# Optimization experiments

Hardware: AMD Instinct MI355X
Metric: run time of the kernel (lower is better)

## Reference

```python
import jax, jax.numpy as jnp
import numpy as np

N, E = 50000, 800000
F_IN, HID, CLS, K = 128, 128, 40, 4


def setup_inputs() -> dict:
    key = jax.random.key(0)
    ks = jax.random.split(key, 6)
    x = jax.random.normal(ks[0], (N, F_IN), jnp.float32)
    edge_src = jax.random.randint(ks[1], (E,), 0, N, jnp.int32)
    edge_dst = jax.random.randint(ks[2], (E,), 0, N, jnp.int32)
    glorot = lambda k, sh, fan: jax.random.normal(k, sh, jnp.float32) * np.float32(1.0 / np.sqrt(fan))
    W0 = glorot(ks[3], (K, F_IN, HID), F_IN)
    W1 = glorot(ks[4], (K, HID, HID), HID)
    W2 = glorot(ks[5], (K, HID, CLS), HID)
    b0 = jnp.zeros((HID,), jnp.float32)
    b1 = jnp.zeros((HID,), jnp.float32)
    b2 = jnp.zeros((CLS,), jnp.float32)
    return dict(x=x, edge_src=edge_src, edge_dst=edge_dst,
                W0=W0, b0=b0, W1=W1, b1=b1, W2=W2, b2=b2)


def _cheb_edge_norm(edge_src, edge_dst, n):
    # PyG ChebConv 'sym' norm with lambda_max=2: scaled Laplacian
    # L_hat = 2L/lambda_max - I = -D^{-1/2} A D^{-1/2}  (diagonal is exactly 0)
    ones = jnp.ones(edge_src.shape[0], jnp.float32)
    deg = jax.ops.segment_sum(ones, edge_src, num_segments=n)
    dinv = jnp.where(deg > 0, jax.lax.rsqrt(jnp.maximum(deg, 1.0)), 0.0)
    return -dinv[edge_src] * dinv[edge_dst]  # [E]


def _cheb_conv(x, edge_src, edge_dst, w_norm, W, b, n):
    # Chebyshev recurrence: Tx0 = x, Tx1 = L_hat x, Tx_k = 2 L_hat Tx_{k-1} - Tx_{k-2}
    def lhat(t):  # SpMM: out[dst] += w * t[src]
        return jax.ops.segment_sum(t[edge_src] * w_norm[:, None], edge_dst, num_segments=n)

    Tx0 = x
    out = Tx0 @ W[0]
    Tx1 = lhat(Tx0)
    out = out + Tx1 @ W[1]
    for k in range(2, W.shape[0]):
        Tx2 = 2.0 * lhat(Tx1) - Tx0
        out = out + Tx2 @ W[k]
        Tx0, Tx1 = Tx1, Tx2
    return out + b


def reference(x, edge_src, edge_dst, W0, b0, W1, b1, W2, b2):
    n = x.shape[0]
    w_norm = _cheb_edge_norm(edge_src, edge_dst, n)
    h = x
    x1 = h
    for W, b in ((W0, b0), (W1, b1), (W2, b2)):
        x1 = _cheb_conv(h, edge_src, edge_dst, w_norm, W, b, n)
        h = jax.nn.relu(x1)  # dropout(p=0.6) is identity in eval mode
    # original returns log_softmax of the LAST conv's pre-activation x1
    return jax.nn.log_softmax(x1, axis=1)
```

## Files before the change

kernel.cpp:

```cpp
#include <hip/hip_runtime.h>
#include <math.h>

#define NN 50000
#define NE 800000
#define FDIM 128
#define CLS 40
#define AW 512
#define RSLOT 64

typedef __attribute__((ext_vector_type(8))) short short8v;
typedef __attribute__((ext_vector_type(8))) unsigned short ushort8v;
typedef __attribute__((ext_vector_type(4))) float f32x4;

__device__ inline float b2f(unsigned short u) {
    union { unsigned int i; float f; } v; v.i = ((unsigned)u) << 16; return v.f;
}
__device__ inline unsigned short f2b(float f) {
    unsigned int x = __float_as_uint(f);
    unsigned int r = (x + 0x7fffu + ((x >> 16) & 1u)) >> 16;
    return (unsigned short)r;
}


__global__ void zero_k(int* degi, int* fill) {
    int i = blockIdx.x * blockDim.x + threadIdx.x;
    if (i < NN) { degi[i] = 0; fill[i] = 0; }
}

#define NB_COUNT 782
#define NB_CVT   3125
#define NB_WH    256
#define NB_WO    96

__global__ __launch_bounds__(256) void prep_k(
        const int4* __restrict__ esrc4,
        int* degi,
        const float* __restrict__ x, unsigned short* __restrict__ Ab,
        const float* __restrict__ W0, const float* __restrict__ W1,
        const float* __restrict__ W2,
        unsigned short* __restrict__ Wt0, unsigned short* __restrict__ Wt1,
        unsigned short* __restrict__ Wt2) {
    int b = blockIdx.x;
    int tid = threadIdx.x;
    if (b < NB_COUNT) {
        int e = b * 256 + tid;
        if (e < NE / 4) {
            int4 s = esrc4[e];
            atomicAdd(&degi[s.x], 1); atomicAdd(&degi[s.y], 1);
            atomicAdd(&degi[s.z], 1); atomicAdd(&degi[s.w], 1);
        }
    } else if (b < NB_COUNT + NB_CVT) {
        int i = (b - NB_COUNT) * 256 + tid;
        int row = i >> 4, cg = i & 15;
        const float4* xp = (const float4*)(x + (size_t)row * FDIM + cg * 8);
        float4 v0 = xp[0], v1 = xp[1];
        ushort8v r;
        r[0] = f2b(v0.x); r[1] = f2b(v0.y); r[2] = f2b(v0.z); r[3] = f2b(v0.w);
        r[4] = f2b(v1.x); r[5] = f2b(v1.y); r[6] = f2b(v1.z); r[7] = f2b(v1.w);
        *(ushort8v*)(Ab + (size_t)row * AW + cg * 8) = r;
    } else if (b < NB_COUNT + NB_CVT + 2 * NB_WH) {
        int wi = b - NB_COUNT - NB_CVT;
        const float* W = (wi < NB_WH) ? W0 : W1;
        unsigned short* Wfm = (wi < NB_WH) ? Wt0 : Wt1;
        int i = (wi % NB_WH) * 256 + tid;
        int j = i & 7, l = (i >> 3) & 63, kcl = (i >> 9) & 3, nt = (i >> 11) & 7, c = i >> 14;
        int r = kcl * 32 + (l >> 4) * 8 + j;
        int col = nt * 16 + (l & 15);
        Wfm[i] = f2b(W[((size_t)c * 128 + r) * 128 + col]);
    } else {
        int i = (b - NB_COUNT - NB_CVT - 2 * NB_WH) * 256 + tid;
        int j = i & 7, l = (i >> 3) & 63, kc = (i >> 9) & 15, nt = i >> 13;
        int k = kc * 32 + (l >> 4) * 8 + j;
        int col = nt * 16 + (l & 15);
        int c = k >> 7, r = k & 127;
        float v = (col < CLS) ? W2[((size_t)c * 128 + r) * CLS + col] : 0.0f;
        Wt2[i] = f2b(v);
    }
}

__global__ void dinv_k(const int* __restrict__ degi, float* __restrict__ dinv) {
    int i = blockIdx.x * blockDim.x + threadIdx.x;
    if (i < NN) {
        int d = degi[i];
        dinv[i] = (d > 0) ? rsqrtf((float)d) : 0.0f;
    }
}

__global__ void scatter_k(const int* __restrict__ esrc, const int* __restrict__ edst,
                          int* fill, const float* __restrict__ dinv,
                          int2* __restrict__ ew) {
    int e = blockIdx.x * blockDim.x + threadIdx.x;
    if (e < NE) {
        int s = esrc[e], d = edst[e];
        int c = atomicAdd(&fill[d], 1);
        if (c < RSLOT) {
            int2 v;
            v.x = s;
            v.y = __float_as_int(-dinv[s] * dinv[d]);
            ew[(size_t)d * RSLOT + c] = v;
        }
    }
}


template <bool CHEB>
__global__ __launch_bounds__(256) void spmm_k(const unsigned short* __restrict__ inp,
                                              const unsigned short* __restrict__ prevp,
                                              unsigned short* __restrict__ outp,
                                              const int* __restrict__ fill,
                                              const int2* __restrict__ ew) {
    int row = blockIdx.x * 4 + (threadIdx.x >> 6);
    int lane = threadIdx.x & 63;
    int slot = lane >> 4, ln = lane & 15;
    int n = fill[row];
    if (n > RSLOT) n = RSLOT;
    int e0 = row * RSLOT, e1 = e0 + n;
    float acc[8] = {0.f, 0.f, 0.f, 0.f, 0.f, 0.f, 0.f, 0.f};
    int e = e0;
    for (; e + 8 <= e1; e += 8) {
        int2 m0 = ew[e + slot * 2];
        int2 m1 = ew[e + slot * 2 + 1];
        ushort8v t0 = *(const ushort8v*)(inp + (size_t)m0.x * AW + ln * 8);
        ushort8v t1 = *(const ushort8v*)(inp + (size_t)m1.x * AW + ln * 8);
        float w0 = __int_as_float(m0.y), w1 = __int_as_float(m1.y);
        #pragma unroll
        for (int j = 0; j < 8; j++)
            acc[j] += w0 * b2f(t0[j]) + w1 * b2f(t1[j]);
    }
    for (; e < e1; e += 4) {
        int ee = e + slot;
        int2 m;
        if (ee < e1) m = ew[ee];
        else { m.x = 0; m.y = 0; }
        ushort8v t = *(const ushort8v*)(inp + (size_t)m.x * AW + ln * 8);
        float w = __int_as_float(m.y);
        #pragma unroll
        for (int j = 0; j < 8; j++) acc[j] += w * b2f(t[j]);
    }
    #pragma unroll
    for (int j = 0; j < 8; j++) {
        acc[j] += __shfl_xor(acc[j], 16);
        acc[j] += __shfl_xor(acc[j], 32);
    }
    if (slot == 0) {
        ushort8v r;
        if (CHEB) {
            ushort8v p = *(const ushort8v*)(prevp + (size_t)row * AW + ln * 8);
            #pragma unroll
            for (int j = 0; j < 8; j++) r[j] = f2b(2.f * acc[j] - b2f(p[j]));
        } else {
            #pragma unroll
            for (int j = 0; j < 8; j++) r[j] = f2b(acc[j]);
        }
        *(ushort8v*)(outp + (size_t)row * AW + ln * 8) = r;
    }
}


__global__ __launch_bounds__(256) void gemm_hid_k(const unsigned short* __restrict__ A,
                                                  const unsigned short* __restrict__ Wfm,
                                                  const float* __restrict__ bias,
                                                  unsigned short* __restrict__ Hout) {
    __shared__ unsigned short Blds[16384];
    int tid = threadIdx.x;
    int w = tid >> 6, lane = tid & 63, ln = lane & 15, gp = lane >> 4;
    int rowbase = blockIdx.x * 64 + w * 16;
    int rowc = rowbase + ln;
    if (rowc >= NN) rowc = NN - 1;
    const unsigned short* Arow = A + (size_t)rowc * AW + gp * 8;

    f32x4 acc[8];
    #pragma unroll
    for (int i = 0; i < 8; i++) acc[i] = (f32x4){0.f, 0.f, 0.f, 0.f};

    short8v acur[4], anxt[4];
    #pragma unroll
    for (int kcl = 0; kcl < 4; kcl++) acur[kcl] = *(const short8v*)(Arow + kcl * 32);
    {
        const ushort8v* g = (const ushort8v*)Wfm;
        ushort8v* s = (ushort8v*)Blds;
        #pragma unroll
        for (int i = 0; i < 8; i++) s[tid + i * 256] = g[tid + i * 256];
    }
    __syncthreads();

    for (int c = 0; c < 4; c++) {
        if (c < 3) {
            #pragma unroll
            for (int kcl = 0; kcl < 4; kcl++)
                anxt[kcl] = *(const short8v*)(Arow + (c + 1) * 128 + kcl * 32);
        }
        #pragma unroll
        for (int kcl = 0; kcl < 4; kcl++) {
            #pragma unroll
            for (int nt = 0; nt < 8; nt++) {
                short8v b = *(const short8v*)&Blds[((nt * 4 + kcl) * 64 + lane) * 8];
                acc[nt] = __builtin_amdgcn_mfma_f32_16x16x32_bf16(acur[kcl], b, acc[nt], 0, 0, 0);
            }
        }
        if (c < 3) {
            __syncthreads();
            const ushort8v* g = (const ushort8v*)(Wfm + (c + 1) * 16384);
            ushort8v* s = (ushort8v*)Blds;
            #pragma unroll
            for (int i = 0; i < 8; i++) s[tid + i * 256] = g[tid + i * 256];
            __syncthreads();
            #pragma unroll
            for (int kcl = 0; kcl < 4; kcl++) acur[kcl] = anxt[kcl];
        }
    }

    if (rowbase < NN) {
        #pragma unroll
        for (int nt = 0; nt < 8; nt++) {
            int col = nt * 16 + ln;
            float bv = bias[col];
            #pragma unroll
            for (int j = 0; j < 4; j++) {
                int r = rowbase + gp * 4 + j;
                Hout[(size_t)r * AW + col] = f2b(fmaxf(acc[nt][j] + bv, 0.0f));
            }
        }
    }
}

__global__ __launch_bounds__(256) void gemm_out_k(const unsigned short* __restrict__ A,
                                                  const unsigned short* __restrict__ Wfm,
                                                  const float* __restrict__ bias,
                                                  float* __restrict__ outb) {
    __shared__ unsigned short Blds[24576];
    int tid = threadIdx.x;
    int w = tid >> 6, lane = tid & 63, ln = lane & 15, gp = lane >> 4;
    int rowbase = blockIdx.x * 64 + w * 16;
    int rowc = rowbase + ln;
    if (rowc >= NN) rowc = NN - 1;
    const unsigned short* Arow = A + (size_t)rowc * AW + gp * 8;

    f32x4 acc[3];
    #pragma unroll
    for (int i = 0; i < 3; i++) acc[i] = (f32x4){0.f, 0.f, 0.f, 0.f};

    {
        const ushort8v* g = (const ushort8v*)Wfm;
        ushort8v* s = (ushort8v*)Blds;
        #pragma unroll
        for (int i = 0; i < 12; i++) s[tid + i * 256] = g[tid + i * 256];
    }
    short8v a0 = *(const short8v*)(Arow);
    short8v a1 = *(const short8v*)(Arow + 32);
    __syncthreads();

    #pragma unroll
    for (int kc = 0; kc < 16; kc++) {
        short8v a = (kc & 1) ? a1 : a0;
        if (kc < 14) {
            if (kc & 1) a1 = *(const short8v*)(Arow + (kc + 2) * 32);
            else        a0 = *(const short8v*)(Arow + (kc + 2) * 32);
        }
        #pragma unroll
        for (int nt = 0; nt < 3; nt++) {
            short8v b = *(const short8v*)&Blds[((nt * 16 + kc) * 64 + lane) * 8];
            acc[nt] = __builtin_amdgcn_mfma_f32_16x16x32_bf16(a, b, acc[nt], 0, 0, 0);
        }
    }

    float b0v = bias[ln], b1v = bias[16 + ln];
    float b2v = (ln < 8) ? bias[32 + ln] : 0.0f;
    #pragma unroll
    for (int j = 0; j < 4; j++) {
        int r = rowbase + gp * 4 + j;
        float v0 = acc[0][j] + b0v;
        float v1 = acc[1][j] + b1v;
        float v2 = (ln < 8) ? (acc[2][j] + b2v) : -INFINITY;
        float m = fmaxf(fmaxf(v0, v1), v2);
        #pragma unroll
        for (int off = 8; off >= 1; off >>= 1) m = fmaxf(m, __shfl_xor(m, off));
        float s = __expf(v0 - m) + __expf(v1 - m) + ((ln < 8) ? __expf(v2 - m) : 0.0f);
        #pragma unroll
        for (int off = 8; off >= 1; off >>= 1) s += __shfl_xor(s, off);
        float ls = logf(s) + m;
        if (rowbase < NN) {
            outb[(size_t)r * CLS + ln] = v0 - ls;
            outb[(size_t)r * CLS + 16 + ln] = v1 - ls;
            if (ln < 8) outb[(size_t)r * CLS + 32 + ln] = v2 - ls;
        }
    }
}


extern "C" void kernel_launch(void* const* d_in, const int* in_sizes, int n_in,
                              void* d_out, int out_size, void* d_ws, size_t ws_size,
                              hipStream_t stream) {
    const float* x    = (const float*)d_in[0];
    const int*   esrc = (const int*)d_in[1];
    const int*   edst = (const int*)d_in[2];
    const float* W0   = (const float*)d_in[3];
    const float* b0   = (const float*)d_in[4];
    const float* W1   = (const float*)d_in[5];
    const float* b1   = (const float*)d_in[6];
    const float* W2   = (const float*)d_in[7];
    const float* b2   = (const float*)d_in[8];
    float* out = (float*)d_out;

    char* p = (char*)d_ws;
    auto alloc = [&](size_t bytes) -> void* {
        void* r = (void*)p;
        p += (bytes + 255) & ~(size_t)255;
        return r;
    };
    unsigned short* Abuf = (unsigned short*)alloc((size_t)NN * AW * 2);
    int2*  ew   = (int2*)alloc((size_t)NN * RSLOT * 8);
    unsigned short* Wt0  = (unsigned short*)alloc((size_t)128 * AW * 2);
    unsigned short* Wt1  = (unsigned short*)alloc((size_t)128 * AW * 2);
    unsigned short* Wt2  = (unsigned short*)alloc((size_t)48 * AW * 2);
    int*   degi = (int*)alloc(NN * 4);
    int*   fill = (int*)alloc(NN * 4);
    float* dinv = (float*)alloc(NN * 4);

    const int TB = 256;
    int gN = (NN + TB - 1) / TB;
    int gE = (NE + TB - 1) / TB;

    zero_k<<<gN, TB, 0, stream>>>(degi, fill);
    prep_k<<<NB_COUNT + NB_CVT + 2 * NB_WH + NB_WO, TB, 0, stream>>>(
        (const int4*)esrc, degi, x, Abuf, W0, W1, W2, Wt0, Wt1, Wt2);
    dinv_k<<<gN, TB, 0, stream>>>(degi, dinv);
    scatter_k<<<gE, TB, 0, stream>>>(esrc, edst, fill, dinv, ew);

    int gSpmm = (NN + 3) / 4;
    int gGemm = (NN + 63) / 64;

    unsigned short* s0 = Abuf + 0 * 128;
    unsigned short* s1 = Abuf + 1 * 128;
    unsigned short* s2 = Abuf + 2 * 128;
    unsigned short* s3 = Abuf + 3 * 128;

    for (int l = 0; l < 3; l++) {
        spmm_k<false><<<gSpmm, TB, 0, stream>>>(s0, nullptr, s1, fill, ew);
        spmm_k<true><<<gSpmm, TB, 0, stream>>>(s1, s0, s2, fill, ew);
        spmm_k<true><<<gSpmm, TB, 0, stream>>>(s2, s1, s3, fill, ew);
        if (l < 2) {
            const unsigned short* Wt = (l == 0) ? Wt0 : Wt1;
            const float* bl = (l == 0) ? b0 : b1;
            gemm_hid_k<<<gGemm, TB, 0, stream>>>(Abuf, Wt, bl, Abuf);
        } else {
            gemm_out_k<<<gGemm, TB, 0, stream>>>(Abuf, Wt2, b2, out);
        }
    }
}
```

Before: 429.0 us.

## Apply last-layer weights before propagation via Clenshaw recurrence and fold edge weights

For the final Chebyshev layer, the hidden features are first projected through all four weight slices (128→4×64 padded) with one MFMA GEMM. The Chebyshev sum is then evaluated with a Clenshaw-style backward recurrence on 64-wide vectors, so the last three SpMMs gather 64 columns instead of 128, and log_softmax is fused into the final SpMM. Separately, the edge scatter is merged into the prep kernel and stores only source indices, recomputing edge weights from dinv at gather time. This removes a kernel launch and halves the edge-list bytes, at the cost of extra dinv lookups per edge and one more bf16 rounding path in the recurrence.

```diff
diff --git a/kernel.cpp b/kernel.cpp
--- a/kernel.cpp
+++ b/kernel.cpp
@@ -6,6 +6,7 @@
 #define FDIM 128
 #define CLS 40
 #define AW 512
+#define ZW 256
 #define RSLOT 64
 
 typedef __attribute__((ext_vector_type(8))) short short8v;
@@ -27,30 +28,38 @@
     if (i < NN) { degi[i] = 0; fill[i] = 0; }
 }
 
-#define NB_COUNT 782
-#define NB_CVT   3125
-#define NB_WH    256
-#define NB_WO    96
+#define NB_ES   782
+#define NB_CVT  3125
+#define NB_WH   256
+#define NB_WZ   128
 
 __global__ __launch_bounds__(256) void prep_k(
-        const int4* __restrict__ esrc4,
-        int* degi,
+        const int4* __restrict__ esrc4, const int4* __restrict__ edst4,
+        int* degi, int* fill, int* __restrict__ ews,
         const float* __restrict__ x, unsigned short* __restrict__ Ab,
         const float* __restrict__ W0, const float* __restrict__ W1,
         const float* __restrict__ W2,
         unsigned short* __restrict__ Wt0, unsigned short* __restrict__ Wt1,
-        unsigned short* __restrict__ Wt2) {
+        unsigned short* __restrict__ Wz) {
     int b = blockIdx.x;
     int tid = threadIdx.x;
-    if (b < NB_COUNT) {
+    if (b < NB_ES) {
         int e = b * 256 + tid;
         if (e < NE / 4) {
-            int4 s = esrc4[e];
+            int4 s = esrc4[e], d = edst4[e];
             atomicAdd(&degi[s.x], 1); atomicAdd(&degi[s.y], 1);
             atomicAdd(&degi[s.z], 1); atomicAdd(&degi[s.w], 1);
-        }
-    } else if (b < NB_COUNT + NB_CVT) {
-        int i = (b - NB_COUNT) * 256 + tid;
+            int c0 = atomicAdd(&fill[d.x], 1);
+            int c1 = atomicAdd(&fill[d.y], 1);
+            int c2 = atomicAdd(&fill[d.z], 1);
+            int c3 = atomicAdd(&fill[d.w], 1);
+            if (c0 < RSLOT) ews[d.x * RSLOT + c0] = s.x;
+            if (c1 < RSLOT) ews[d.y * RSLOT + c1] = s.y;
+            if (c2 < RSLOT) ews[d.z * RSLOT + c2] = s.z;
+            if (c3 < RSLOT) ews[d.w * RSLOT + c3] = s.w;
+        }
+    } else if (b < NB_ES + NB_CVT) {
+        int i = (b - NB_ES) * 256 + tid;
         int row = i >> 4, cg = i & 15;
         const float4* xp = (const float4*)(x + (size_t)row * FDIM + cg * 8);
         float4 v0 = xp[0], v1 = xp[1];
@@ -58,8 +67,8 @@
         r[0] = f2b(v0.x); r[1] = f2b(v0.y); r[2] = f2b(v0.z); r[3] = f2b(v0.w);
         r[4] = f2b(v1.x); r[5] = f2b(v1.y); r[6] = f2b(v1.z); r[7] = f2b(v1.w);
         *(ushort8v*)(Ab + (size_t)row * AW + cg * 8) = r;
-    } else if (b < NB_COUNT + NB_CVT + 2 * NB_WH) {
-        int wi = b - NB_COUNT - NB_CVT;
+    } else if (b < NB_ES + NB_CVT + 2 * NB_WH) {
+        int wi = b - NB_ES - NB_CVT;
         const float* W = (wi < NB_WH) ? W0 : W1;
         unsigned short* Wfm = (wi < NB_WH) ? Wt0 : Wt1;
         int i = (wi % NB_WH) * 256 + tid;
@@ -68,13 +77,13 @@
         int col = nt * 16 + (l & 15);
         Wfm[i] = f2b(W[((size_t)c * 128 + r) * 128 + col]);
     } else {
-        int i = (b - NB_COUNT - NB_CVT - 2 * NB_WH) * 256 + tid;
-        int j = i & 7, l = (i >> 3) & 63, kc = (i >> 9) & 15, nt = i >> 13;
-        int k = kc * 32 + (l >> 4) * 8 + j;
-        int col = nt * 16 + (l & 15);
-        int c = k >> 7, r = k & 127;
-        float v = (col < CLS) ? W2[((size_t)c * 128 + r) * CLS + col] : 0.0f;
-        Wt2[i] = f2b(v);
+        int i = (b - NB_ES - NB_CVT - 2 * NB_WH) * 256 + tid;
+        int j = i & 7, l = (i >> 3) & 63, kcl = (i >> 9) & 3, nt = (i >> 11) & 7, half = (i >> 14) & 1;
+        int k = kcl * 32 + (l >> 4) * 8 + j;
+        int col = half * 128 + nt * 16 + (l & 15);
+        int kcheb = col >> 6, cc = col & 63;
+        float v = (cc < CLS) ? W2[((size_t)kcheb * 128 + k) * CLS + cc] : 0.0f;
+        Wz[i] = f2b(v);
     }
 }
 
@@ -86,54 +95,37 @@
     }
 }
 
-__global__ void scatter_k(const int* __restrict__ esrc, const int* __restrict__ edst,
-                          int* fill, const float* __restrict__ dinv,
-                          int2* __restrict__ ew) {
-    int e = blockIdx.x * blockDim.x + threadIdx.x;
-    if (e < NE) {
-        int s = esrc[e], d = edst[e];
-        int c = atomicAdd(&fill[d], 1);
-        if (c < RSLOT) {
-            int2 v;
-            v.x = s;
-            v.y = __float_as_int(-dinv[s] * dinv[d]);
-            ew[(size_t)d * RSLOT + c] = v;
-        }
-    }
-}
-
 
 template <bool CHEB>
 __global__ __launch_bounds__(256) void spmm_k(const unsigned short* __restrict__ inp,
                                               const unsigned short* __restrict__ prevp,
                                               unsigned short* __restrict__ outp,
                                               const int* __restrict__ fill,
-                                              const int2* __restrict__ ew) {
+                                              const int* __restrict__ ews,
+                                              const float* __restrict__ dinv) {
     int row = blockIdx.x * 4 + (threadIdx.x >> 6);
     int lane = threadIdx.x & 63;
     int slot = lane >> 4, ln = lane & 15;
     int n = fill[row];
     if (n > RSLOT) n = RSLOT;
     int e0 = row * RSLOT, e1 = e0 + n;
+    float dvr = dinv[row];
     float acc[8] = {0.f, 0.f, 0.f, 0.f, 0.f, 0.f, 0.f, 0.f};
     int e = e0;
     for (; e + 8 <= e1; e += 8) {
-        int2 m0 = ew[e + slot * 2];
-        int2 m1 = ew[e + slot * 2 + 1];
-        ushort8v t0 = *(const ushort8v*)(inp + (size_t)m0.x * AW + ln * 8);
-        ushort8v t1 = *(const ushort8v*)(inp + (size_t)m1.x * AW + ln * 8);
-        float w0 = __int_as_float(m0.y), w1 = __int_as_float(m1.y);
+        int2 s01 = *(const int2*)&ews[e + slot * 2];
+        ushort8v t0 = *(const ushort8v*)(inp + (size_t)s01.x * AW + ln * 8);
+        ushort8v t1 = *(const ushort8v*)(inp + (size_t)s01.y * AW + ln * 8);
+        float w0 = -dinv[s01.x] * dvr, w1 = -dinv[s01.y] * dvr;
         #pragma unroll
         for (int j = 0; j < 8; j++)
             acc[j] += w0 * b2f(t0[j]) + w1 * b2f(t1[j]);
     }
     for (; e < e1; e += 4) {
         int ee = e + slot;
-        int2 m;
-        if (ee < e1) m = ew[ee];
-        else { m.x = 0; m.y = 0; }
-        ushort8v t = *(const ushort8v*)(inp + (size_t)m.x * AW + ln * 8);
-        float w = __int_as_float(m.y);
+        int s = (ee < e1) ? ews[ee] : 0;
+        float w = (ee < e1) ? (-dinv[s] * dvr) : 0.0f;
+        ushort8v t = *(const ushort8v*)(inp + (size_t)s * AW + ln * 8);
         #pragma unroll
         for (int j = 0; j < 8; j++) acc[j] += w * b2f(t[j]);
     }
@@ -153,6 +145,87 @@
             for (int j = 0; j < 8; j++) r[j] = f2b(acc[j]);
         }
         *(ushort8v*)(outp + (size_t)row * AW + ln * 8) = r;
+    }
+}
+
+
+template <int MODE>
+__global__ __launch_bounds__(256) void spmm64_k(const unsigned short* __restrict__ gsrc,
+                                                const unsigned short* __restrict__ zadd,
+                                                const unsigned short* __restrict__ bsub,
+                                                unsigned short* __restrict__ wout,
+                                                float* __restrict__ fout,
+                                                const int* __restrict__ fill,
+                                                const int* __restrict__ ews,
+                                                const float* __restrict__ dinv) {
+    constexpr int GS = (MODE == 0) ? ZW : 64;
+    constexpr float SC = (MODE == 2) ? 1.0f : 2.0f;
+    int row = blockIdx.x * 4 + (threadIdx.x >> 6);
+    int lane = threadIdx.x & 63;
+    int slot = lane >> 3, ln = lane & 7;
+    int n = fill[row];
+    if (n > RSLOT) n = RSLOT;
+    int e0 = row * RSLOT, e1 = e0 + n;
+    float dvr = dinv[row];
+    float acc[8] = {0.f, 0.f, 0.f, 0.f, 0.f, 0.f, 0.f, 0.f};
+    int e = e0;
+    for (; e + 16 <= e1; e += 16) {
+        int2 s01 = *(const int2*)&ews[e + slot * 2];
+        ushort8v t0 = *(const ushort8v*)(gsrc + (size_t)s01.x * GS + ln * 8);
+        ushort8v t1 = *(const ushort8v*)(gsrc + (size_t)s01.y * GS + ln * 8);
+        float w0 = -dinv[s01.x] * dvr, w1 = -dinv[s01.y] * dvr;
+        #pragma unroll
+        for (int j = 0; j < 8; j++)
+            acc[j] += w0 * b2f(t0[j]) + w1 * b2f(t1[j]);
+    }
+    for (; e < e1; e += 8) {
+        int ee = e + slot;
+        int s = (ee < e1) ? ews[ee] : 0;
+        float w = (ee < e1) ? (-dinv[s] * dvr) : 0.0f;
+        ushort8v t = *(const ushort8v*)(gsrc + (size_t)s * GS + ln * 8);
+        #pragma unroll
+        for (int j = 0; j < 8; j++) acc[j] += w * b2f(t[j]);
+    }
+    #pragma unroll
+    for (int j = 0; j < 8; j++) {
+        acc[j] += __shfl_xor(acc[j], 8);
+        acc[j] += __shfl_xor(acc[j], 16);
+        acc[j] += __shfl_xor(acc[j], 32);
+    }
+    if (slot != 0) return;
+    ushort8v zv = *(const ushort8v*)(zadd + (size_t)row * ZW + ln * 8);
+    float v[8];
+    if (MODE == 0) {
+        #pragma unroll
+        for (int j = 0; j < 8; j++) v[j] = b2f(zv[j]) + SC * acc[j];
+    } else {
+        constexpr int BS = (MODE == 1) ? ZW : 64;
+        ushort8v bv = *(const ushort8v*)(bsub + (size_t)row * BS + ln * 8);
+        #pragma unroll
+        for (int j = 0; j < 8; j++) v[j] = b2f(zv[j]) + SC * acc[j] - b2f(bv[j]);
+    }
+    if (MODE < 2) {
+        ushort8v r;
+        #pragma unroll
+        for (int j = 0; j < 8; j++) r[j] = f2b(v[j]);
+        *(ushort8v*)(wout + (size_t)row * 64 + ln * 8) = r;
+    } else {
+        float m = -INFINITY;
+        #pragma unroll
+        for (int j = 0; j < 8; j++) if (ln * 8 + j < CLS) m = fmaxf(m, v[j]);
+        #pragma unroll
+        for (int off = 4; off >= 1; off >>= 1) m = fmaxf(m, __shfl_xor(m, off));
+        float s = 0.f;
+        #pragma unroll
+        for (int j = 0; j < 8; j++) if (ln * 8 + j < CLS) s += __expf(v[j] - m);
+        #pragma unroll
+        for (int off = 4; off >= 1; off >>= 1) s += __shfl_xor(s, off);
+        float ls = logf(s) + m;
+        #pragma unroll
+        for (int j = 0; j < 8; j++) {
+            int col = ln * 8 + j;
+            if (col < CLS) fout[(size_t)row * CLS + col] = v[j] - ls;
+        }
     }
 }
 
@@ -224,11 +297,12 @@
     }
 }
 
-__global__ __launch_bounds__(256) void gemm_out_k(const unsigned short* __restrict__ A,
-                                                  const unsigned short* __restrict__ Wfm,
-                                                  const float* __restrict__ bias,
-                                                  float* __restrict__ outb) {
-    __shared__ unsigned short Blds[24576];
+
+__global__ __launch_bounds__(256) void gemm_z_k(const unsigned short* __restrict__ A,
+                                                const unsigned short* __restrict__ Wz,
+                                                const float* __restrict__ b2,
+                                                unsigned short* __restrict__ Z) {
+    __shared__ unsigned short Blds[16384];
     int tid = threadIdx.x;
     int w = tid >> 6, lane = tid & 63, ln = lane & 15, gp = lane >> 4;
     int rowbase = blockIdx.x * 64 + w * 16;
@@ -236,53 +310,41 @@
     if (rowc >= NN) rowc = NN - 1;
     const unsigned short* Arow = A + (size_t)rowc * AW + gp * 8;
 
-    f32x4 acc[3];
+    short8v af[4];
     #pragma unroll
-    for (int i = 0; i < 3; i++) acc[i] = (f32x4){0.f, 0.f, 0.f, 0.f};
-
-    {
-        const ushort8v* g = (const ushort8v*)Wfm;
-        ushort8v* s = (ushort8v*)Blds;
-        #pragma unroll
-        for (int i = 0; i < 12; i++) s[tid + i * 256] = g[tid + i * 256];
-    }
-    short8v a0 = *(const short8v*)(Arow);
-    short8v a1 = *(const short8v*)(Arow + 32);
-    __syncthreads();
-
-    #pragma unroll
-    for (int kc = 0; kc < 16; kc++) {
-        short8v a = (kc & 1) ? a1 : a0;
-        if (kc < 14) {
-            if (kc & 1) a1 = *(const short8v*)(Arow + (kc + 2) * 32);
-            else        a0 = *(const short8v*)(Arow + (kc + 2) * 32);
-        }
-        #pragma unroll
-        for (int nt = 0; nt < 3; nt++) {
-            short8v b = *(const short8v*)&Blds[((nt * 16 + kc) * 64 + lane) * 8];
-            acc[nt] = __builtin_amdgcn_mfma_f32_16x16x32_bf16(a, b, acc[nt], 0, 0, 0);
-        }
-    }
-
-    float b0v = bias[ln], b1v = bias[16 + ln];
-    float b2v = (ln < 8) ? bias[32 + ln] : 0.0f;
-    #pragma unroll
-    for (int j = 0; j < 4; j++) {
-        int r = rowbase + gp * 4 + j;
-        float v0 = acc[0][j] + b0v;
-        float v1 = acc[1][j] + b1v;
-        float v2 = (ln < 8) ? (acc[2][j] + b2v) : -INFINITY;
-        float m = fmaxf(fmaxf(v0, v1), v2);
-        #pragma unroll
-        for (int off = 8; off >= 1; off >>= 1) m = fmaxf(m, __shfl_xor(m, off));
-        float s = __expf(v0 - m) + __expf(v1 - m) + ((ln < 8) ? __expf(v2 - m) : 0.0f);
-        #pragma unroll
-        for (int off = 8; off >= 1; off >>= 1) s += __shfl_xor(s, off);
-        float ls = logf(s) + m;
+    for (int kcl = 0; kcl < 4; kcl++) af[kcl] = *(const short8v*)(Arow + kcl * 32);
+
+    for (int half = 0; half < 2; half++) {
+        if (half) __syncthreads();
+        {
+            const ushort8v* g = (const ushort8v*)(Wz + half * 16384);
+            ushort8v* s = (ushort8v*)Blds;
+            #pragma unroll
+            for (int i = 0; i < 8; i++) s[tid + i * 256] = g[tid + i * 256];
+        }
+        __syncthreads();
+        f32x4 acc[8];
+        #pragma unroll
+        for (int i = 0; i < 8; i++) acc[i] = (f32x4){0.f, 0.f, 0.f, 0.f};
+        #pragma unroll
+        for (int kcl = 0; kcl < 4; kcl++) {
+            #pragma unroll
+            for (int nt = 0; nt < 8; nt++) {
+                short8v b = *(const short8v*)&Blds[((nt * 4 + kcl) * 64 + lane) * 8];
+                acc[nt] = __builtin_amdgcn_mfma_f32_16x16x32_bf16(af[kcl], b, acc[nt], 0, 0, 0);
+            }
+        }
         if (rowbase < NN) {
-            outb[(size_t)r * CLS + ln] = v0 - ls;
-            outb[(size_t)r * CLS + 16 + ln] = v1 - ls;
-            if (ln < 8) outb[(size_t)r * CLS + 32 + ln] = v2 - ls;
+            #pragma unroll
+            for (int nt = 0; nt < 8; nt++) {
+                int col = half * 128 + nt * 16 + ln;
+                float bv = (col < CLS) ? b2[col] : 0.0f;
+                #pragma unroll
+                for (int j = 0; j < 4; j++) {
+                    int r = rowbase + gp * 4 + j;
+                    Z[(size_t)r * ZW + col] = f2b(acc[nt][j] + bv);
+                }
+            }
         }
     }
 }
@@ -309,23 +371,25 @@
         return r;
     };
     unsigned short* Abuf = (unsigned short*)alloc((size_t)NN * AW * 2);
-    int2*  ew   = (int2*)alloc((size_t)NN * RSLOT * 8);
+    unsigned short* Zbuf = (unsigned short*)alloc((size_t)NN * ZW * 2);
+    unsigned short* B1b  = (unsigned short*)alloc((size_t)NN * 64 * 2);
+    unsigned short* B2b  = (unsigned short*)alloc((size_t)NN * 64 * 2);
+    int*   ews  = (int*)alloc((size_t)NN * RSLOT * 4);
     unsigned short* Wt0  = (unsigned short*)alloc((size_t)128 * AW * 2);
     unsigned short* Wt1  = (unsigned short*)alloc((size_t)128 * AW * 2);
-    unsigned short* Wt2  = (unsigned short*)alloc((size_t)48 * AW * 2);
+    unsigned short* Wz   = (unsigned short*)alloc((size_t)32768 * 2);
     int*   degi = (int*)alloc(NN * 4);
     int*   fill = (int*)alloc(NN * 4);
     float* dinv = (float*)alloc(NN * 4);
 
     const int TB = 256;
     int gN = (NN + TB - 1) / TB;
-    int gE = (NE + TB - 1) / TB;
 
     zero_k<<<gN, TB, 0, stream>>>(degi, fill);
-    prep_k<<<NB_COUNT + NB_CVT + 2 * NB_WH + NB_WO, TB, 0, stream>>>(
-        (const int4*)esrc, degi, x, Abuf, W0, W1, W2, Wt0, Wt1, Wt2);
+    prep_k<<<NB_ES + NB_CVT + 2 * NB_WH + NB_WZ, TB, 0, stream>>>(
+        (const int4*)esrc, (const int4*)edst, degi, fill, ews,
+        x, Abuf, W0, W1, W2, Wt0, Wt1, Wz);
     dinv_k<<<gN, TB, 0, stream>>>(degi, dinv);
-    scatter_k<<<gE, TB, 0, stream>>>(esrc, edst, fill, dinv, ew);
 
     int gSpmm = (NN + 3) / 4;
     int gGemm = (NN + 63) / 64;
@@ -335,16 +399,20 @@
     unsigned short* s2 = Abuf + 2 * 128;
     unsigned short* s3 = Abuf + 3 * 128;
 
-    for (int l = 0; l < 3; l++) {
-        spmm_k<false><<<gSpmm, TB, 0, stream>>>(s0, nullptr, s1, fill, ew);
-        spmm_k<true><<<gSpmm, TB, 0, stream>>>(s1, s0, s2, fill, ew);
-        spmm_k<true><<<gSpmm, TB, 0, stream>>>(s2, s1, s3, fill, ew);
-        if (l < 2) {
-            const unsigned short* Wt = (l == 0) ? Wt0 : Wt1;
-            const float* bl = (l == 0) ? b0 : b1;
-            gemm_hid_k<<<gGemm, TB, 0, stream>>>(Abuf, Wt, bl, Abuf);
-        } else {
-            gemm_out_k<<<gGemm, TB, 0, stream>>>(Abuf, Wt2, b2, out);
-        }
-    }
-}
+    for (int l = 0; l < 2; l++) {
+        spmm_k<false><<<gSpmm, TB, 0, stream>>>(s0, nullptr, s1, fill, ews, dinv);
+        spmm_k<true><<<gSpmm, TB, 0, stream>>>(s1, s0, s2, fill, ews, dinv);
+        spmm_k<true><<<gSpmm, TB, 0, stream>>>(s2, s1, s3, fill, ews, dinv);
+        const unsigned short* Wt = (l == 0) ? Wt0 : Wt1;
+        const float* bl = (l == 0) ? b0 : b1;
+        gemm_hid_k<<<gGemm, TB, 0, stream>>>(Abuf, Wt, bl, Abuf);
+    }
+
+    gemm_z_k<<<gGemm, TB, 0, stream>>>(Abuf, Wz, b2, Zbuf);
+    spmm64_k<0><<<gSpmm, TB, 0, stream>>>(Zbuf + 192, Zbuf + 128, nullptr,
+                                          B2b, nullptr, fill, ews, dinv);
+    spmm64_k<1><<<gSpmm, TB, 0, stream>>>(B2b, Zbuf + 64, Zbuf + 192,
+                                          B1b, nullptr, fill, ews, dinv);
+    spmm64_k<2><<<gSpmm, TB, 0, stream>>>(B1b, Zbuf, B2b,
+                                          nullptr, out, fill, ews, dinv);
+}
```

Measured after the change: 427.5 us. About the same (-0.3%).
